# Kernel optimization log

Hardware: AMD Instinct MI355X
Metric: run time of the kernel (lower is better)

## Reference

```python
import jax, jax.numpy as jnp
import numpy as np

N = 100000      # nodes
E = 1600000     # edges (avg degree 16)
DIN, DH, DOUT = 128, 64, 32


def setup_inputs() -> dict:
    key = jax.random.key(0)
    ks = jax.random.split(key, 6)
    x = jax.random.normal(ks[0], (N, DIN), dtype=jnp.float32)
    edge_index = jax.random.randint(ks[1], (2, E), 0, N, dtype=jnp.int32)
    # GCNConv weights (glorot-ish scale), biases zero-init as in PyG default
    W1 = jax.random.normal(ks[2], (DIN, DH), dtype=jnp.float32) / np.sqrt(DIN).astype(np.float32)
    b1 = jnp.zeros((DH,), dtype=jnp.float32)
    W2 = jax.random.normal(ks[3], (DH, DOUT), dtype=jnp.float32) / np.sqrt(DH).astype(np.float32)
    b2 = jnp.zeros((DOUT,), dtype=jnp.float32)
    # fc is hard-reset in reset_parameters: weight=ones, bias=zeros
    fc_w = jnp.ones((1, DOUT), dtype=jnp.float32)
    fc_b = jnp.zeros((1,), dtype=jnp.float32)
    return {"x": x, "edge_index": edge_index, "W1": W1, "b1": b1,
            "W2": W2, "b2": b2, "fc_w": fc_w, "fc_b": fc_b}


def gcn_conv(x, W, b, src, dst, n):
    """PyG GCNConv: add self-loops, symmetric deg normalization, x@W then aggregate."""
    h = x @ W                                             # [n, dout] transform first
    ones = jnp.ones(src.shape[0], dtype=x.dtype)
    deg = jax.ops.segment_sum(ones, dst, num_segments=n) + 1.0   # +1 for self-loop
    dinv = jax.lax.rsqrt(deg)
    coef = dinv[src] * dinv[dst]                          # [E] edge norm
    agg = jax.ops.segment_sum(h[src] * coef[:, None], dst, num_segments=n)
    agg = agg + h * (1.0 / deg)[:, None]                  # self-loop term: dinv_i*dinv_i
    return agg + b


def reference(x, edge_index, W1, b1, W2, b2, fc_w, fc_b):
    src, dst = edge_index[0], edge_index[1]
    h = jax.nn.relu(gcn_conv(x, W1, b1, src, dst, N))
    h = jax.nn.relu(gcn_conv(h, W2, b2, src, dst, N))
    scores = (h @ fc_w.T + fc_b)[:, 0]                    # Linear(out,1) then squeeze
    return scores, h
```

## Files before the change

### kernel.cpp

```cpp
#include <hip/hip_runtime.h>

#define NN 100000
#define EE 1600000
#define DIN 128
#define DH 64
#define DOUT 32

#define BSH 8
#define BNODES 256
#define NBUCK ((NN + BNODES - 1) / BNODES)
#define BCAP 4608
#define CHUNK 4096
#define NCHUNK ((EE + CHUNK - 1) / CHUNK)

typedef unsigned short ush;
typedef __attribute__((ext_vector_type(8))) short bf16x8;
typedef __attribute__((ext_vector_type(4))) float f32x4;

__device__ __forceinline__ float bflo(unsigned u) {
    union { unsigned u; float f; } c; c.u = u << 16; return c.f;
}
__device__ __forceinline__ float bfhi(unsigned u) {
    union { unsigned u; float f; } c; c.u = u & 0xffff0000u; return c.f;
}
__device__ __forceinline__ ush f2bf(float f) {
    union { float f; unsigned u; } c; c.f = f;
    unsigned r = c.u + 0x7fff + ((c.u >> 16) & 1);
    return (ush)(r >> 16);
}

__global__ void init_bcur_kernel(int* __restrict__ bcur) {
    int i = blockIdx.x * 256 + threadIdx.x;
    if (i < NBUCK) bcur[i] = i * BCAP;
}

__global__ __launch_bounds__(256) void binA_kernel(const int* __restrict__ src,
                                                   const int* __restrict__ dst,
                                                   int* __restrict__ bcur,
                                                   unsigned* __restrict__ tmp) {
    __shared__ int hist[NBUCK];
    __shared__ int scn[NBUCK];
    __shared__ int cur[NBUCK];
    __shared__ int gb[NBUCK];
    __shared__ int s2[256];
    __shared__ unsigned staged[CHUNK];
    __shared__ int gaddr[CHUNK];
    int t = threadIdx.x;
    for (int i = t; i < NBUCK; i += 256) hist[i] = 0;
    __syncthreads();
    int e0 = blockIdx.x * CHUNK;
    int nE = min(CHUNK, EE - e0);

    int my_e[16], my_bk[16];
#pragma unroll
    for (int k = 0; k < 16; k++) {
        int li = t + k * 256;
        bool ok = li < nE;
        int idx = ok ? (e0 + li) : e0;
        int d = dst[idx];
        int s = src[idx];
        int b = d >> BSH;
        my_e[k] = (s << 8) | (d & 255);
        my_bk[k] = ok ? b : -1;
        if (ok) atomicAdd(&hist[b], 1);
    }
    __syncthreads();
    int a0 = (2 * t < NBUCK) ? hist[2 * t] : 0;
    int a1 = (2 * t + 1 < NBUCK) ? hist[2 * t + 1] : 0;
    s2[t] = a0 + a1;
    __syncthreads();
    for (int off = 1; off < 256; off <<= 1) {
        int x = (t >= off) ? s2[t - off] : 0;
        __syncthreads();
        s2[t] += x;
        __syncthreads();
    }
    int excl = s2[t] - a0 - a1;
    if (2 * t < NBUCK)     { scn[2 * t] = excl;          cur[2 * t] = excl; }
    if (2 * t + 1 < NBUCK) { scn[2 * t + 1] = excl + a0; cur[2 * t + 1] = excl + a0; }
    __syncthreads();
    for (int i = t; i < NBUCK; i += 256) {
        int h = hist[i];
        if (h) gb[i] = atomicAdd(&bcur[i], h) - scn[i];
    }
    __syncthreads();
#pragma unroll
    for (int k = 0; k < 16; k++) {
        int b = my_bk[k];
        if (b >= 0) {
            int lp = atomicAdd(&cur[b], 1);
            staged[lp] = (unsigned)my_e[k];
            gaddr[lp] = gb[b] + lp;
        }
    }
    __syncthreads();
    for (int i = t; i < nE; i += 256)
        tmp[gaddr[i]] = staged[i];
}

__global__ __launch_bounds__(256) void binB_kernel(const unsigned* __restrict__ tmp,
                                                   const int* __restrict__ bcur,
                                                   int* __restrict__ csr,
                                                   int* __restrict__ offs,
                                                   int* __restrict__ ends,
                                                   float* __restrict__ dinv) {
    __shared__ int hist[BNODES], cur[BNODES], sc[BNODES];
    int b = blockIdx.x, t = threadIdx.x;
    int e0 = b * BCAP, e1 = bcur[b];
    hist[t] = 0;
    __syncthreads();
    for (int i = e0 + t; i < e1; i += 256) atomicAdd(&hist[tmp[i] & 255], 1);
    __syncthreads();
    int v = hist[t];
    sc[t] = v;
    __syncthreads();
    for (int off = 1; off < 256; off <<= 1) {
        int x = (t >= off) ? sc[t - off] : 0;
        __syncthreads();
        sc[t] += x;
        __syncthreads();
    }
    int excl = sc[t] - v;
    cur[t] = e0 + excl;
    int node = (b << BSH) + t;
    if (node < NN) {
        offs[node] = e0 + excl;
        ends[node] = e0 + excl + v;
        dinv[node] = 1.0f / sqrtf((float)v + 1.0f);
    }
    __syncthreads();
    for (int i = e0 + t; i < e1; i += 256) {
        unsigned u = tmp[i];
        int pos = atomicAdd(&cur[u & 255], 1);
        csr[pos] = (int)(u >> 8);
    }
}

template <int K, int NC, typename XT>
__global__ __launch_bounds__(256) void gemm_mfma_kernel(const XT* __restrict__ X,
                                                        const float* __restrict__ W,
                                                        const float* __restrict__ dinv,
                                                        ush* __restrict__ Y) {
    constexpr int GROWS = 128;
    constexpr int KP = K + 8;
    constexpr int NKC = K / 32;
    constexpr int NCT = NC / 16;
    __shared__ __align__(16) ush Xl[GROWS * KP];
    __shared__ __align__(16) ush Wt[NC * KP];
    const int t = threadIdx.x;
    const int row0 = blockIdx.x * GROWS;

    if constexpr (sizeof(XT) == 4) {
        for (int i = t; i < GROWS * (K / 4); i += 256) {
            int r = i / (K / 4), c4 = i % (K / 4);
            int row = row0 + r;
            float4 v = make_float4(0.f, 0.f, 0.f, 0.f);
            if (row < NN) v = *(const float4*)&X[(size_t)row * K + c4 * 4];
            ushort4 o;
            o.x = f2bf(v.x); o.y = f2bf(v.y); o.z = f2bf(v.z); o.w = f2bf(v.w);
            *(ushort4*)&Xl[r * KP + c4 * 4] = o;
        }
    } else {
        for (int i = t; i < GROWS * (K / 8); i += 256) {
            int r = i / (K / 8), c8 = i % (K / 8);
            int row = row0 + r;
            uint4 v = make_uint4(0, 0, 0, 0);
            if (row < NN) v = *(const uint4*)&X[(size_t)row * K + c8 * 8];
            *(uint4*)&Xl[r * KP + c8 * 8] = v;
        }
    }
    for (int i = t; i < K * (NC / 4); i += 256) {
        int k = i / (NC / 4), n4 = i % (NC / 4);
        float4 v = *(const float4*)&W[k * NC + n4 * 4];
        Wt[(n4 * 4 + 0) * KP + k] = f2bf(v.x);
        Wt[(n4 * 4 + 1) * KP + k] = f2bf(v.y);
        Wt[(n4 * 4 + 2) * KP + k] = f2bf(v.z);
        Wt[(n4 * 4 + 3) * KP + k] = f2bf(v.w);
    }
    __syncthreads();

    const int wave = t >> 6, lane = t & 63;
    const int m = lane & 15, quad = lane >> 4;
    const int wrow = wave * 32;

    f32x4 acc[2][NCT];
#pragma unroll
    for (int rt = 0; rt < 2; rt++)
#pragma unroll
        for (int ct = 0; ct < NCT; ct++) acc[rt][ct] = (f32x4){0.f, 0.f, 0.f, 0.f};

#pragma unroll
    for (int kc = 0; kc < NKC; kc++) {
        int koff = kc * 32 + quad * 8;
        bf16x8 b[NCT];
#pragma unroll
        for (int ct = 0; ct < NCT; ct++)
            b[ct] = *(const bf16x8*)&Wt[(ct * 16 + m) * KP + koff];
#pragma unroll
        for (int rt = 0; rt < 2; rt++) {
            bf16x8 a = *(const bf16x8*)&Xl[(wrow + rt * 16 + m) * KP + koff];
#pragma unroll
            for (int ct = 0; ct < NCT; ct++)
                acc[rt][ct] = __builtin_amdgcn_mfma_f32_16x16x32_bf16(a, b[ct], acc[rt][ct], 0, 0, 0);
        }
    }
#pragma unroll
    for (int rt = 0; rt < 2; rt++) {
#pragma unroll
        for (int reg = 0; reg < 4; reg++) {
            int row = row0 + wrow + rt * 16 + quad * 4 + reg;
            if (row < NN) {
                float s = dinv[row];
#pragma unroll
                for (int ct = 0; ct < NCT; ct++)
                    Y[(size_t)row * NC + ct * 16 + m] = f2bf(acc[rt][ct][reg] * s);
            }
        }
    }
}

#define ACC8(u4)                                      \
    acc0 += bflo(u4.x); acc1 += bfhi(u4.x);           \
    acc2 += bflo(u4.y); acc3 += bfhi(u4.y);           \
    acc4 += bflo(u4.z); acc5 += bfhi(u4.z);           \
    acc6 += bflo(u4.w); acc7 += bfhi(u4.w);

__global__ __launch_bounds__(256) void gather1_kernel(const int* __restrict__ offs,
                                                      const int* __restrict__ ends,
                                                      const float* __restrict__ dinv,
                                                      const ush* __restrict__ Hs,
                                                      const int* __restrict__ csr,
                                                      const float* __restrict__ b1,
                                                      ush* __restrict__ h1) {
    int wid = (blockIdx.x * 256 + threadIdx.x) >> 6;
    int lane = threadIdx.x & 63;
    int node = wid * 2 + (lane >> 5);
    if (node >= NN) return;
    int l = lane & 31;
    int es = l >> 3;
    int fg = l & 7;
    int start = offs[node], end = ends[node];
    float dv = dinv[node];
    uint4 su = *(const uint4*)&Hs[node * DH + fg * 8];
    float acc0 = 0.f, acc1 = 0.f, acc2 = 0.f, acc3 = 0.f;
    float acc4 = 0.f, acc5 = 0.f, acc6 = 0.f, acc7 = 0.f;
    int k = start + es;
    for (; k + 12 < end; k += 16) {
        int s0 = csr[k], s1 = csr[k + 4], s2 = csr[k + 8], s3 = csr[k + 12];
        uint4 u0 = *(const uint4*)&Hs[s0 * DH + fg * 8];
        uint4 u1 = *(const uint4*)&Hs[s1 * DH + fg * 8];
        uint4 u2 = *(const uint4*)&Hs[s2 * DH + fg * 8];
        uint4 u3 = *(const uint4*)&Hs[s3 * DH + fg * 8];
        ACC8(u0) ACC8(u1) ACC8(u2) ACC8(u3)
    }
    for (; k < end; k += 4) {
        int s = csr[k];
        uint4 u = *(const uint4*)&Hs[s * DH + fg * 8];
        ACC8(u)
    }
#pragma unroll
    for (int m = 8; m <= 16; m <<= 1) {
        acc0 += __shfl_xor(acc0, m); acc1 += __shfl_xor(acc1, m);
        acc2 += __shfl_xor(acc2, m); acc3 += __shfl_xor(acc3, m);
        acc4 += __shfl_xor(acc4, m); acc5 += __shfl_xor(acc5, m);
        acc6 += __shfl_xor(acc6, m); acc7 += __shfl_xor(acc7, m);
    }
    float4 ba = *(const float4*)&b1[fg * 8];
    float4 bb = *(const float4*)&b1[fg * 8 + 4];
    if (es == 0) {
        ushort4 o0, o1;
        o0.x = f2bf(fmaxf(dv * (acc0 + bflo(su.x)) + ba.x, 0.f));
        o0.y = f2bf(fmaxf(dv * (acc1 + bfhi(su.x)) + ba.y, 0.f));
        o0.z = f2bf(fmaxf(dv * (acc2 + bflo(su.y)) + ba.z, 0.f));
        o0.w = f2bf(fmaxf(dv * (acc3 + bfhi(su.y)) + ba.w, 0.f));
        o1.x = f2bf(fmaxf(dv * (acc4 + bflo(su.z)) + bb.x, 0.f));
        o1.y = f2bf(fmaxf(dv * (acc5 + bfhi(su.z)) + bb.y, 0.f));
        o1.z = f2bf(fmaxf(dv * (acc6 + bflo(su.w)) + bb.z, 0.f));
        o1.w = f2bf(fmaxf(dv * (acc7 + bfhi(su.w)) + bb.w, 0.f));
        *(ushort4*)&h1[node * DH + fg * 8] = o0;
        *(ushort4*)&h1[node * DH + fg * 8 + 4] = o1;
    }
}

__global__ __launch_bounds__(256) void gather2_kernel(const int* __restrict__ offs,
                                                      const int* __restrict__ ends,
                                                      const float* __restrict__ dinv,
                                                      const ush* __restrict__ Hs,
                                                      const int* __restrict__ csr,
                                                      const float* __restrict__ b2,
                                                      const float* __restrict__ fcw,
                                                      const float* __restrict__ fcb,
                                                      float* __restrict__ h2,
                                                      float* __restrict__ scores) {
    int wid = (blockIdx.x * 256 + threadIdx.x) >> 6;
    int lane = threadIdx.x & 63;
    int node = wid * 2 + (lane >> 5);
    if (node >= NN) return;
    int l = lane & 31;
    int es = l >> 2;
    int fg = l & 3;
    int start = offs[node], end = ends[node];
    float dv = dinv[node];
    uint4 su = *(const uint4*)&Hs[node * DOUT + fg * 8];
    float acc0 = 0.f, acc1 = 0.f, acc2 = 0.f, acc3 = 0.f;
    float acc4 = 0.f, acc5 = 0.f, acc6 = 0.f, acc7 = 0.f;
    int k = start + es;
    for (; k + 8 < end; k += 16) {
        int s0 = csr[k], s1 = csr[k + 8];
        uint4 u0 = *(const uint4*)&Hs[s0 * DOUT + fg * 8];
        uint4 u1 = *(const uint4*)&Hs[s1 * DOUT + fg * 8];
        ACC8(u0) ACC8(u1)
    }
    for (; k < end; k += 8) {
        int s = csr[k];
        uint4 u = *(const uint4*)&Hs[s * DOUT + fg * 8];
        ACC8(u)
    }
#pragma unroll
    for (int m = 4; m <= 16; m <<= 1) {
        acc0 += __shfl_xor(acc0, m); acc1 += __shfl_xor(acc1, m);
        acc2 += __shfl_xor(acc2, m); acc3 += __shfl_xor(acc3, m);
        acc4 += __shfl_xor(acc4, m); acc5 += __shfl_xor(acc5, m);
        acc6 += __shfl_xor(acc6, m); acc7 += __shfl_xor(acc7, m);
    }
    float4 ba = *(const float4*)&b2[fg * 8];
    float4 bb = *(const float4*)&b2[fg * 8 + 4];
    float4 o0, o1;
    o0.x = fmaxf(dv * (acc0 + bflo(su.x)) + ba.x, 0.f);
    o0.y = fmaxf(dv * (acc1 + bfhi(su.x)) + ba.y, 0.f);
    o0.z = fmaxf(dv * (acc2 + bflo(su.y)) + ba.z, 0.f);
    o0.w = fmaxf(dv * (acc3 + bfhi(su.y)) + ba.w, 0.f);
    o1.x = fmaxf(dv * (acc4 + bflo(su.z)) + bb.x, 0.f);
    o1.y = fmaxf(dv * (acc5 + bfhi(su.z)) + bb.y, 0.f);
    o1.z = fmaxf(dv * (acc6 + bflo(su.w)) + bb.z, 0.f);
    o1.w = fmaxf(dv * (acc7 + bfhi(su.w)) + bb.w, 0.f);
    if (es == 0) {
        *(float4*)&h2[node * DOUT + fg * 8] = o0;
        *(float4*)&h2[node * DOUT + fg * 8 + 4] = o1;
    }
    float4 fa = *(const float4*)&fcw[fg * 8];
    float4 fb = *(const float4*)&fcw[fg * 8 + 4];
    float sv = o0.x * fa.x + o0.y * fa.y + o0.z * fa.z + o0.w * fa.w
             + o1.x * fb.x + o1.y * fb.y + o1.z * fb.z + o1.w * fb.w;
    sv += __shfl_xor(sv, 1); sv += __shfl_xor(sv, 2);
    if (l == 0) scores[node] = sv + fcb[0];
}

extern "C" void kernel_launch(void* const* d_in, const int* in_sizes, int n_in,
                              void* d_out, int out_size, void* d_ws, size_t ws_size,
                              hipStream_t stream) {
    const float* x   = (const float*)d_in[0];
    const int*   ei  = (const int*)d_in[1];
    const float* W1  = (const float*)d_in[2];
    const float* b1  = (const float*)d_in[3];
    const float* W2  = (const float*)d_in[4];
    const float* b2  = (const float*)d_in[5];
    const float* fcw = (const float*)d_in[6];
    const float* fcb = (const float*)d_in[7];
    const int* src = ei;
    const int* dst = ei + EE;

    float* ws = (float*)d_ws;
    float* dinv    = ws;
    int*   offs    = (int*)(ws + 100352);
    int*   ends    = (int*)(ws + 200704);
    int*   bcur    = (int*)(ws + 301056);
    int*   csr     = (int*)(ws + 301568);
    unsigned* tmp  = (unsigned*)(ws + 2103296);
    ush*   Hs1     = (ush*)(ws + 3905024);
    ush*   Hs2     = (ush*)(ws + 7105024);
    ush*   h1      = (ush*)(ws + 8705024);

    float* out    = (float*)d_out;
    float* scores = out;
    float* h2     = out + NN;

    const int T = 256;
    init_bcur_kernel<<<2, 256, 0, stream>>>(bcur);
    binA_kernel<<<NCHUNK, T, 0, stream>>>(src, dst, bcur, tmp);
    binB_kernel<<<NBUCK, T, 0, stream>>>(tmp, bcur, csr, offs, ends, dinv);
    gemm_mfma_kernel<DIN, DH, float><<<(NN + 127) / 128, T, 0, stream>>>(x, W1, dinv, Hs1);
    gather1_kernel<<<(NN / 2 * 64 + T - 1) / T, T, 0, stream>>>(offs, ends, dinv, Hs1, csr, b1, h1);
    gemm_mfma_kernel<DH, DOUT, ush><<<(NN + 127) / 128, T, 0, stream>>>(h1, W2, dinv, Hs2);
    gather2_kernel<<<(NN / 2 * 64 + T - 1) / T, T, 0, stream>>>(offs, ends, dinv, Hs2, csr, b2, fcw, fcb, h2, scores);
}
```

Measured before the change: 225.5 us.

## Fuse layer-2 weight transform into layer-1 gather epilogue

```diff
diff --git a/kernel.cpp b/kernel.cpp
--- a/kernel.cpp
+++ b/kernel.cpp
@@ -225,13 +225,29 @@
     acc4 += bflo(u4.z); acc5 += bfhi(u4.z);           \
     acc6 += bflo(u4.w); acc7 += bfhi(u4.w);
 
-__global__ __launch_bounds__(256) void gather1_kernel(const int* __restrict__ offs,
-                                                      const int* __restrict__ ends,
-                                                      const float* __restrict__ dinv,
-                                                      const ush* __restrict__ Hs,
-                                                      const int* __restrict__ csr,
-                                                      const float* __restrict__ b1,
-                                                      ush* __restrict__ h1) {
+__global__ __launch_bounds__(256) void gather1_fused_kernel(const int* __restrict__ offs,
+                                                            const int* __restrict__ ends,
+                                                            const float* __restrict__ dinv,
+                                                            const ush* __restrict__ Hs,
+                                                            const int* __restrict__ csr,
+                                                            const float* __restrict__ b1,
+                                                            const float* __restrict__ W2,
+                                                            ush* __restrict__ Hs2) {
+    __shared__ ush W2l[DH * DOUT];
+    {
+        int i = threadIdx.x;
+        int row = i >> 2, cb = i & 3;
+        int cbs = cb ^ ((row >> 3) & 3);
+        float4 va = *(const float4*)&W2[row * DOUT + cb * 8];
+        float4 vb = *(const float4*)&W2[row * DOUT + cb * 8 + 4];
+        ushort4 oa, ob;
+        oa.x = f2bf(va.x); oa.y = f2bf(va.y); oa.z = f2bf(va.z); oa.w = f2bf(va.w);
+        ob.x = f2bf(vb.x); ob.y = f2bf(vb.y); ob.z = f2bf(vb.z); ob.w = f2bf(vb.w);
+        *(ushort4*)&W2l[row * DOUT + cbs * 8] = oa;
+        *(ushort4*)&W2l[row * DOUT + cbs * 8 + 4] = ob;
+    }
+    __syncthreads();
+
     int wid = (blockIdx.x * 256 + threadIdx.x) >> 6;
     int lane = threadIdx.x & 63;
     int node = wid * 2 + (lane >> 5);
@@ -267,18 +283,39 @@
     }
     float4 ba = *(const float4*)&b1[fg * 8];
     float4 bb = *(const float4*)&b1[fg * 8 + 4];
-    if (es == 0) {
-        ushort4 o0, o1;
-        o0.x = f2bf(fmaxf(dv * (acc0 + bflo(su.x)) + ba.x, 0.f));
-        o0.y = f2bf(fmaxf(dv * (acc1 + bfhi(su.x)) + ba.y, 0.f));
-        o0.z = f2bf(fmaxf(dv * (acc2 + bflo(su.y)) + ba.z, 0.f));
-        o0.w = f2bf(fmaxf(dv * (acc3 + bfhi(su.y)) + ba.w, 0.f));
-        o1.x = f2bf(fmaxf(dv * (acc4 + bflo(su.z)) + bb.x, 0.f));
-        o1.y = f2bf(fmaxf(dv * (acc5 + bfhi(su.z)) + bb.y, 0.f));
-        o1.z = f2bf(fmaxf(dv * (acc6 + bflo(su.w)) + bb.z, 0.f));
-        o1.w = f2bf(fmaxf(dv * (acc7 + bfhi(su.w)) + bb.w, 0.f));
-        *(ushort4*)&h1[node * DH + fg * 8] = o0;
-        *(ushort4*)&h1[node * DH + fg * 8 + 4] = o1;
+    float h[8];
+    h[0] = fmaxf(dv * (acc0 + bflo(su.x)) + ba.x, 0.f);
+    h[1] = fmaxf(dv * (acc1 + bfhi(su.x)) + ba.y, 0.f);
+    h[2] = fmaxf(dv * (acc2 + bflo(su.y)) + ba.z, 0.f);
+    h[3] = fmaxf(dv * (acc3 + bfhi(su.y)) + ba.w, 0.f);
+    h[4] = fmaxf(dv * (acc4 + bflo(su.z)) + bb.x, 0.f);
+    h[5] = fmaxf(dv * (acc5 + bfhi(su.z)) + bb.y, 0.f);
+    h[6] = fmaxf(dv * (acc6 + bflo(su.w)) + bb.z, 0.f);
+    h[7] = fmaxf(dv * (acc7 + bfhi(su.w)) + bb.w, 0.f);
+#pragma unroll
+    for (int r = 0; r < 8; r++) h[r] = bflo((unsigned)f2bf(h[r]));
+    const int jb = es * 8;
+    float p[8] = {0.f, 0.f, 0.f, 0.f, 0.f, 0.f, 0.f, 0.f};
+#pragma unroll
+    for (int r = 0; r < 8; r++) {
+        bf16x8 w = *(const bf16x8*)&W2l[(fg * 8 + r) * DOUT + (jb ^ ((fg & 3) << 3))];
+#pragma unroll
+        for (int c = 0; c < 8; c++)
+            p[c] += h[r] * bflo((unsigned)(ush)w[c]);
+    }
+#pragma unroll
+    for (int m = 1; m <= 4; m <<= 1) {
+#pragma unroll
+        for (int c = 0; c < 8; c++) p[c] += __shfl_xor(p[c], m);
+    }
+    if (fg == 0) {
+        ushort4 oa, ob;
+        oa.x = f2bf(p[0] * dv); oa.y = f2bf(p[1] * dv);
+        oa.z = f2bf(p[2] * dv); oa.w = f2bf(p[3] * dv);
+        ob.x = f2bf(p[4] * dv); ob.y = f2bf(p[5] * dv);
+        ob.z = f2bf(p[6] * dv); ob.w = f2bf(p[7] * dv);
+        *(ushort4*)&Hs2[node * DOUT + jb] = oa;
+        *(ushort4*)&Hs2[node * DOUT + jb + 4] = ob;
     }
 }
 
@@ -369,7 +406,6 @@
     unsigned* tmp  = (unsigned*)(ws + 2103296);
     ush*   Hs1     = (ush*)(ws + 3905024);
     ush*   Hs2     = (ush*)(ws + 7105024);
-    ush*   h1      = (ush*)(ws + 8705024);
 
     float* out    = (float*)d_out;
     float* scores = out;
@@ -380,7 +416,6 @@
     binA_kernel<<<NCHUNK, T, 0, stream>>>(src, dst, bcur, tmp);
     binB_kernel<<<NBUCK, T, 0, stream>>>(tmp, bcur, csr, offs, ends, dinv);
     gemm_mfma_kernel<DIN, DH, float><<<(NN + 127) / 128, T, 0, stream>>>(x, W1, dinv, Hs1);
-    gather1_kernel<<<(NN / 2 * 64 + T - 1) / T, T, 0, stream>>>(offs, ends, dinv, Hs1, csr, b1, h1);
-    gemm_mfma_kernel<DH, DOUT, ush><<<(NN + 127) / 128, T, 0, stream>>>(h1, W2, dinv, Hs2);
+    gather1_fused_kernel<<<(NN / 2 * 64 + T - 1) / T, T, 0, stream>>>(offs, ends, dinv, Hs1, csr, b1, W2, Hs2);
     gather2_kernel<<<(NN / 2 * 64 + T - 1) / T, T, 0, stream>>>(offs, ends, dinv, Hs2, csr, b2, fcw, fcb, h2, scores);
 }
```

Result: no change. 225.2 us (-0.1%).

## Fuse layer-2 GEMM into layer-1 gather epilogue and use packed FP32 math

Applied to the files above, without the earlier changes.

```diff
diff --git a/kernel.cpp b/kernel.cpp
--- a/kernel.cpp
+++ b/kernel.cpp
@@ -16,6 +16,7 @@
 typedef unsigned short ush;
 typedef __attribute__((ext_vector_type(8))) short bf16x8;
 typedef __attribute__((ext_vector_type(4))) float f32x4;
+typedef __attribute__((ext_vector_type(2))) float f32x2;
 
 __device__ __forceinline__ float bflo(unsigned u) {
     union { unsigned u; float f; } c; c.u = u << 16; return c.f;
@@ -27,6 +28,19 @@
     union { float f; unsigned u; } c; c.f = f;
     unsigned r = c.u + 0x7fff + ((c.u >> 16) & 1);
     return (ush)(r >> 16);
+}
+
+__device__ __forceinline__ void pka(f32x2& a, f32x2 b) {
+    asm("v_pk_add_f32 %0, %0, %1" : "+v"(a) : "v"(b));
+}
+__device__ __forceinline__ void pkfma(f32x2& d, f32x2 a, f32x2 b) {
+    asm("v_pk_fma_f32 %0, %1, %2, %0" : "+v"(d) : "v"(a), "v"(b));
+}
+__device__ __forceinline__ void pkmul(f32x2& a, f32x2 b) {
+    asm("v_pk_mul_f32 %0, %0, %1" : "+v"(a) : "v"(b));
+}
+__device__ __forceinline__ f32x2 up2(unsigned u) {
+    f32x2 p; p.x = bflo(u); p.y = bfhi(u); return p;
 }
 
 __global__ void init_bcur_kernel(int* __restrict__ bcur) {
@@ -219,19 +233,35 @@
     }
 }
 
-#define ACC8(u4)                                      \
-    acc0 += bflo(u4.x); acc1 += bfhi(u4.x);           \
-    acc2 += bflo(u4.y); acc3 += bfhi(u4.y);           \
-    acc4 += bflo(u4.z); acc5 += bfhi(u4.z);           \
-    acc6 += bflo(u4.w); acc7 += bfhi(u4.w);
-
-__global__ __launch_bounds__(256) void gather1_kernel(const int* __restrict__ offs,
-                                                      const int* __restrict__ ends,
-                                                      const float* __restrict__ dinv,
-                                                      const ush* __restrict__ Hs,
-                                                      const int* __restrict__ csr,
-                                                      const float* __restrict__ b1,
-                                                      ush* __restrict__ h1) {
+#define ACCP(u4) { pka(ac0, up2(u4.x)); pka(ac1, up2(u4.y)); \
+                   pka(ac2, up2(u4.z)); pka(ac3, up2(u4.w)); }
+
+#define BFLY(msk) { f32x2 t_;                                           \
+    t_.x = __shfl_xor(ac0.x, msk); t_.y = __shfl_xor(ac0.y, msk); pka(ac0, t_); \
+    t_.x = __shfl_xor(ac1.x, msk); t_.y = __shfl_xor(ac1.y, msk); pka(ac1, t_); \
+    t_.x = __shfl_xor(ac2.x, msk); t_.y = __shfl_xor(ac2.y, msk); pka(ac2, t_); \
+    t_.x = __shfl_xor(ac3.x, msk); t_.y = __shfl_xor(ac3.y, msk); pka(ac3, t_); }
+
+__global__ __launch_bounds__(256) void gather1_fused_kernel(const int* __restrict__ offs,
+                                                            const int* __restrict__ ends,
+                                                            const float* __restrict__ dinv,
+                                                            const ush* __restrict__ Hs,
+                                                            const int* __restrict__ csr,
+                                                            const float* __restrict__ b1,
+                                                            const float* __restrict__ W2,
+                                                            ush* __restrict__ Hs2) {
+    __shared__ __align__(16) float Wp[32 * 68];
+    {
+        int t = threadIdx.x;
+        int lp = t >> 3, r = t & 7;
+        int srow = (lp & 7) * 8 + r, scol = (lp >> 3) * 8;
+        float4 va = *(const float4*)&W2[srow * DOUT + scol];
+        float4 vb = *(const float4*)&W2[srow * DOUT + scol + 4];
+        *(float4*)&Wp[lp * 68 + r * 8] = va;
+        *(float4*)&Wp[lp * 68 + r * 8 + 4] = vb;
+    }
+    __syncthreads();
+
     int wid = (blockIdx.x * 256 + threadIdx.x) >> 6;
     int lane = threadIdx.x & 63;
     int node = wid * 2 + (lane >> 5);
@@ -242,8 +272,7 @@
     int start = offs[node], end = ends[node];
     float dv = dinv[node];
     uint4 su = *(const uint4*)&Hs[node * DH + fg * 8];
-    float acc0 = 0.f, acc1 = 0.f, acc2 = 0.f, acc3 = 0.f;
-    float acc4 = 0.f, acc5 = 0.f, acc6 = 0.f, acc7 = 0.f;
+    f32x2 ac0 = {0.f, 0.f}, ac1 = {0.f, 0.f}, ac2 = {0.f, 0.f}, ac3 = {0.f, 0.f};
     int k = start + es;
     for (; k + 12 < end; k += 16) {
         int s0 = csr[k], s1 = csr[k + 4], s2 = csr[k + 8], s3 = csr[k + 12];
@@ -251,34 +280,59 @@
         uint4 u1 = *(const uint4*)&Hs[s1 * DH + fg * 8];
         uint4 u2 = *(const uint4*)&Hs[s2 * DH + fg * 8];
         uint4 u3 = *(const uint4*)&Hs[s3 * DH + fg * 8];
-        ACC8(u0) ACC8(u1) ACC8(u2) ACC8(u3)
+        ACCP(u0) ACCP(u1) ACCP(u2) ACCP(u3)
     }
     for (; k < end; k += 4) {
         int s = csr[k];
         uint4 u = *(const uint4*)&Hs[s * DH + fg * 8];
-        ACC8(u)
-    }
-#pragma unroll
-    for (int m = 8; m <= 16; m <<= 1) {
-        acc0 += __shfl_xor(acc0, m); acc1 += __shfl_xor(acc1, m);
-        acc2 += __shfl_xor(acc2, m); acc3 += __shfl_xor(acc3, m);
-        acc4 += __shfl_xor(acc4, m); acc5 += __shfl_xor(acc5, m);
-        acc6 += __shfl_xor(acc6, m); acc7 += __shfl_xor(acc7, m);
-    }
+        ACCP(u)
+    }
+    BFLY(8) BFLY(16)
+
     float4 ba = *(const float4*)&b1[fg * 8];
     float4 bb = *(const float4*)&b1[fg * 8 + 4];
-    if (es == 0) {
-        ushort4 o0, o1;
-        o0.x = f2bf(fmaxf(dv * (acc0 + bflo(su.x)) + ba.x, 0.f));
-        o0.y = f2bf(fmaxf(dv * (acc1 + bfhi(su.x)) + ba.y, 0.f));
-        o0.z = f2bf(fmaxf(dv * (acc2 + bflo(su.y)) + ba.z, 0.f));
-        o0.w = f2bf(fmaxf(dv * (acc3 + bfhi(su.y)) + ba.w, 0.f));
-        o1.x = f2bf(fmaxf(dv * (acc4 + bflo(su.z)) + bb.x, 0.f));
-        o1.y = f2bf(fmaxf(dv * (acc5 + bfhi(su.z)) + bb.y, 0.f));
-        o1.z = f2bf(fmaxf(dv * (acc6 + bflo(su.w)) + bb.z, 0.f));
-        o1.w = f2bf(fmaxf(dv * (acc7 + bfhi(su.w)) + bb.w, 0.f));
-        *(ushort4*)&h1[node * DH + fg * 8] = o0;
-        *(ushort4*)&h1[node * DH + fg * 8 + 4] = o1;
+    f32x2 dvp; dvp.x = dv; dvp.y = dv;
+    pka(ac0, up2(su.x)); pka(ac1, up2(su.y)); pka(ac2, up2(su.z)); pka(ac3, up2(su.w));
+    f32x2 h0; h0.x = ba.x; h0.y = ba.y;
+    f32x2 h1; h1.x = ba.z; h1.y = ba.w;
+    f32x2 h2; h2.x = bb.x; h2.y = bb.y;
+    f32x2 h3; h3.x = bb.z; h3.y = bb.w;
+    pkfma(h0, dvp, ac0); pkfma(h1, dvp, ac1); pkfma(h2, dvp, ac2); pkfma(h3, dvp, ac3);
+    h0.x = fmaxf(h0.x, 0.f); h0.y = fmaxf(h0.y, 0.f);
+    h1.x = fmaxf(h1.x, 0.f); h1.y = fmaxf(h1.y, 0.f);
+    h2.x = fmaxf(h2.x, 0.f); h2.y = fmaxf(h2.y, 0.f);
+    h3.x = fmaxf(h3.x, 0.f); h3.y = fmaxf(h3.y, 0.f);
+
+    const float* wl = &Wp[l * 68];
+    float hs_[8] = {h0.x, h0.y, h1.x, h1.y, h2.x, h2.y, h3.x, h3.y};
+    f32x2 p0 = {0.f, 0.f}, p1 = {0.f, 0.f}, p2 = {0.f, 0.f}, p3 = {0.f, 0.f};
+#pragma unroll
+    for (int r = 0; r < 8; r++) {
+        float4 wa = *(const float4*)&wl[r * 8];
+        float4 wb = *(const float4*)&wl[r * 8 + 4];
+        f32x2 hr; hr.x = hs_[r]; hr.y = hs_[r];
+        f32x2 w01; w01.x = wa.x; w01.y = wa.y;
+        f32x2 w23; w23.x = wa.z; w23.y = wa.w;
+        f32x2 w45; w45.x = wb.x; w45.y = wb.y;
+        f32x2 w67; w67.x = wb.z; w67.y = wb.w;
+        pkfma(p0, hr, w01); pkfma(p1, hr, w23);
+        pkfma(p2, hr, w45); pkfma(p3, hr, w67);
+    }
+#pragma unroll
+    for (int msk = 1; msk <= 4; msk <<= 1) {
+        f32x2 t_;
+        t_.x = __shfl_xor(p0.x, msk); t_.y = __shfl_xor(p0.y, msk); pka(p0, t_);
+        t_.x = __shfl_xor(p1.x, msk); t_.y = __shfl_xor(p1.y, msk); pka(p1, t_);
+        t_.x = __shfl_xor(p2.x, msk); t_.y = __shfl_xor(p2.y, msk); pka(p2, t_);
+        t_.x = __shfl_xor(p3.x, msk); t_.y = __shfl_xor(p3.y, msk); pka(p3, t_);
+    }
+    if (fg == 0) {
+        pkmul(p0, dvp); pkmul(p1, dvp); pkmul(p2, dvp); pkmul(p3, dvp);
+        ushort4 oa, ob;
+        oa.x = f2bf(p0.x); oa.y = f2bf(p0.y); oa.z = f2bf(p1.x); oa.w = f2bf(p1.y);
+        ob.x = f2bf(p2.x); ob.y = f2bf(p2.y); ob.z = f2bf(p3.x); ob.w = f2bf(p3.y);
+        *(ushort4*)&Hs2[node * DOUT + es * 8] = oa;
+        *(ushort4*)&Hs2[node * DOUT + es * 8 + 4] = ob;
     }
 }
 
@@ -302,46 +356,50 @@
     int start = offs[node], end = ends[node];
     float dv = dinv[node];
     uint4 su = *(const uint4*)&Hs[node * DOUT + fg * 8];
-    float acc0 = 0.f, acc1 = 0.f, acc2 = 0.f, acc3 = 0.f;
-    float acc4 = 0.f, acc5 = 0.f, acc6 = 0.f, acc7 = 0.f;
+    f32x2 ac0 = {0.f, 0.f}, ac1 = {0.f, 0.f}, ac2 = {0.f, 0.f}, ac3 = {0.f, 0.f};
     int k = start + es;
     for (; k + 8 < end; k += 16) {
         int s0 = csr[k], s1 = csr[k + 8];
         uint4 u0 = *(const uint4*)&Hs[s0 * DOUT + fg * 8];
         uint4 u1 = *(const uint4*)&Hs[s1 * DOUT + fg * 8];
-        ACC8(u0) ACC8(u1)
+        ACCP(u0) ACCP(u1)
     }
     for (; k < end; k += 8) {
         int s = csr[k];
         uint4 u = *(const uint4*)&Hs[s * DOUT + fg * 8];
-        ACC8(u)
-    }
-#pragma unroll
-    for (int m = 4; m <= 16; m <<= 1) {
-        acc0 += __shfl_xor(acc0, m); acc1 += __shfl_xor(acc1, m);
-        acc2 += __shfl_xor(acc2, m); acc3 += __shfl_xor(acc3, m);
-        acc4 += __shfl_xor(acc4, m); acc5 += __shfl_xor(acc5, m);
-        acc6 += __shfl_xor(acc6, m); acc7 += __shfl_xor(acc7, m);
-    }
+        ACCP(u)
+    }
+    BFLY(4) BFLY(8) BFLY(16)
+
     float4 ba = *(const float4*)&b2[fg * 8];
     float4 bb = *(const float4*)&b2[fg * 8 + 4];
-    float4 o0, o1;
-    o0.x = fmaxf(dv * (acc0 + bflo(su.x)) + ba.x, 0.f);
-    o0.y = fmaxf(dv * (acc1 + bfhi(su.x)) + ba.y, 0.f);
-    o0.z = fmaxf(dv * (acc2 + bflo(su.y)) + ba.z, 0.f);
-    o0.w = fmaxf(dv * (acc3 + bfhi(su.y)) + ba.w, 0.f);
-    o1.x = fmaxf(dv * (acc4 + bflo(su.z)) + bb.x, 0.f);
-    o1.y = fmaxf(dv * (acc5 + bfhi(su.z)) + bb.y, 0.f);
-    o1.z = fmaxf(dv * (acc6 + bflo(su.w)) + bb.z, 0.f);
-    o1.w = fmaxf(dv * (acc7 + bfhi(su.w)) + bb.w, 0.f);
+    f32x2 dvp; dvp.x = dv; dvp.y = dv;
+    pka(ac0, up2(su.x)); pka(ac1, up2(su.y)); pka(ac2, up2(su.z)); pka(ac3, up2(su.w));
+    f32x2 h0; h0.x = ba.x; h0.y = ba.y;
+    f32x2 h1; h1.x = ba.z; h1.y = ba.w;
+    f32x2 h2v; h2v.x = bb.x; h2v.y = bb.y;
+    f32x2 h3; h3.x = bb.z; h3.y = bb.w;
+    pkfma(h0, dvp, ac0); pkfma(h1, dvp, ac1); pkfma(h2v, dvp, ac2); pkfma(h3, dvp, ac3);
+    h0.x = fmaxf(h0.x, 0.f); h0.y = fmaxf(h0.y, 0.f);
+    h1.x = fmaxf(h1.x, 0.f); h1.y = fmaxf(h1.y, 0.f);
+    h2v.x = fmaxf(h2v.x, 0.f); h2v.y = fmaxf(h2v.y, 0.f);
+    h3.x = fmaxf(h3.x, 0.f); h3.y = fmaxf(h3.y, 0.f);
     if (es == 0) {
+        float4 o0, o1;
+        o0.x = h0.x; o0.y = h0.y; o0.z = h1.x; o0.w = h1.y;
+        o1.x = h2v.x; o1.y = h2v.y; o1.z = h3.x; o1.w = h3.y;
         *(float4*)&h2[node * DOUT + fg * 8] = o0;
         *(float4*)&h2[node * DOUT + fg * 8 + 4] = o1;
     }
     float4 fa = *(const float4*)&fcw[fg * 8];
     float4 fb = *(const float4*)&fcw[fg * 8 + 4];
-    float sv = o0.x * fa.x + o0.y * fa.y + o0.z * fa.z + o0.w * fa.w
-             + o1.x * fb.x + o1.y * fb.y + o1.z * fb.z + o1.w * fb.w;
+    f32x2 dp = {0.f, 0.f};
+    f32x2 f01; f01.x = fa.x; f01.y = fa.y;
+    f32x2 f23; f23.x = fa.z; f23.y = fa.w;
+    f32x2 f45; f45.x = fb.x; f45.y = fb.y;
+    f32x2 f67; f67.x = fb.z; f67.y = fb.w;
+    pkfma(dp, h0, f01); pkfma(dp, h1, f23); pkfma(dp, h2v, f45); pkfma(dp, h3, f67);
+    float sv = dp.x + dp.y;
     sv += __shfl_xor(sv, 1); sv += __shfl_xor(sv, 2);
     if (l == 0) scores[node] = sv + fcb[0];
 }
@@ -369,7 +427,6 @@
     unsigned* tmp  = (unsigned*)(ws + 2103296);
     ush*   Hs1     = (ush*)(ws + 3905024);
     ush*   Hs2     = (ush*)(ws + 7105024);
-    ush*   h1      = (ush*)(ws + 8705024);
 
     float* out    = (float*)d_out;
     float* scores = out;
@@ -380,7 +437,6 @@
     binA_kernel<<<NCHUNK, T, 0, stream>>>(src, dst, bcur, tmp);
     binB_kernel<<<NBUCK, T, 0, stream>>>(tmp, bcur, csr, offs, ends, dinv);
     gemm_mfma_kernel<DIN, DH, float><<<(NN + 127) / 128, T, 0, stream>>>(x, W1, dinv, Hs1);
-    gather1_kernel<<<(NN / 2 * 64 + T - 1) / T, T, 0, stream>>>(offs, ends, dinv, Hs1, csr, b1, h1);
-    gemm_mfma_kernel<DH, DOUT, ush><<<(NN + 127) / 128, T, 0, stream>>>(h1, W2, dinv, Hs2);
+    gather1_fused_kernel<<<(NN / 2 * 64 + T - 1) / T, T, 0, stream>>>(offs, ends, dinv, Hs1, csr, b1, W2, Hs2);
     gather2_kernel<<<(NN / 2 * 64 + T - 1) / T, T, 0, stream>>>(offs, ends, dinv, Hs2, csr, b2, fcw, fcb, h2, scores);
 }
```

After: 229.0 us. Within noise of the previous version (+1.6%).
